# Kernel optimization log

Measured on AMD Instinct MI355X. Metric: run time of the kernel, lower is better.

## Reference

```python
import jax, jax.numpy as jnp
import numpy as np

VOCAB = 100000
DIM = 300
SEQ = 200
BATCH = 1024


def setup_inputs() -> dict:
    key = jax.random.key(0)
    ks = jax.random.split(key, 7)
    tokens = jax.random.randint(ks[0], (SEQ, BATCH), 0, VOCAB, dtype=jnp.int32)
    static_lut = jax.random.normal(ks[1], (VOCAB, DIM), dtype=jnp.float32)
    # lut = pretrained vectors + N(0, 0.01) noise
    lut = static_lut + 0.01 * jax.random.normal(ks[2], (VOCAB, DIM), dtype=jnp.float32)
    W1 = jax.random.normal(ks[3], (600, 600), dtype=jnp.float32) / np.sqrt(600.0)
    b1 = jnp.zeros((600,), dtype=jnp.float32)
    W2 = jax.random.normal(ks[4], (1, 600), dtype=jnp.float32) / np.sqrt(600.0)
    b2 = jnp.zeros((1,), dtype=jnp.float32)
    return {"tokens": tokens, "lut": lut, "static_lut": static_lut,
            "W1": W1, "b1": b1, "W2": W2, "b2": b2}


def _first_occurrence_mask(tokens):
    # tokens: [S, B]. mask[i, b] = 1 iff tokens[i, b] is the first occurrence
    # of that token value in column b (emulates per-column set() dedup).
    S = tokens.shape[0]
    eq = tokens[:, None, :] == tokens[None, :, :]          # [S, S, B]
    first_idx = jnp.argmax(eq, axis=1)                      # [S, B] first j with same token
    return (first_idx == jnp.arange(S, dtype=first_idx.dtype)[:, None])


def reference(tokens, lut, static_lut, W1, b1, W2, b2):
    mask = _first_occurrence_mask(tokens).astype(lut.dtype)  # [S, B]
    # dedup embedding-bag sums over unique tokens per column
    e_learn = jnp.einsum('sbd,sb->bd', lut[tokens], mask)          # [B, 300]
    e_static = jnp.einsum('sbd,sb->bd', static_lut[tokens], mask)  # [B, 300]
    hidden = jnp.concatenate([e_learn, e_static], axis=-1)         # [B, 600]
    h = jax.nn.relu(hidden @ W1.T + b1)                            # [B, 600]
    out = h @ W2.T + b2                                            # [B, 1]
    return out[:, 0]                                               # [B]
```

## Files before the change

### kernel.cpp

```cpp
#include <hip/hip_runtime.h>
#include <limits.h>

#define SEQ   200
#define BATCH 1024
#define DIM   300
#define HID   600
#define VOCAB 100000

#define NQ    4

#define BW    4
#define JCH   12
#define JPER  (HID / JCH)

#define HIDDEN_ELEMS (BATCH * HID)
#define HIDDEN_BYTES ((size_t)HIDDEN_ELEMS * 4)

#define SORT_BYTES  ((size_t)BATCH * 256 * 4)
#define NK_BYTES    ((size_t)BATCH * 4)
#define OFF_NK      SORT_BYTES
#define OFF_HID4    (SORT_BYTES + 65536)
#define OFF_HIDDEN  (OFF_HID4 + 4 * HIDDEN_BYTES)

__global__ __launch_bounds__(256) void sort_kernel(
    const int* __restrict__ tokens,
    int* __restrict__ sorted_g,
    int* __restrict__ nk_g) {
  const int b   = blockIdx.x;
  const int tid = threadIdx.x;

  __shared__ int toks[SEQ];
  __shared__ int stok[256];
  __shared__ int nk_sh;

  for (int s = tid; s < SEQ; s += 256) toks[s] = tokens[s * BATCH + b];
  if (tid == 0) nk_sh = 0;
  __syncthreads();

  int my = INT_MAX;
  if (tid < SEQ) {
    const int t = toks[tid];
    bool k = true;
    for (int p = 0; p < tid; ++p) {
      if (toks[p] == t) { k = false; break; }
    }
    if (k) my = t;
  }
  stok[tid] = my;
  if (my != INT_MAX) atomicAdd(&nk_sh, 1);
  __syncthreads();

  for (int k = 2; k <= 256; k <<= 1) {
    for (int j = k >> 1; j > 0; j >>= 1) {
      const int ixj = tid ^ j;
      if (ixj > tid) {
        const int a = stok[tid];
        const int c = stok[ixj];
        const bool up = ((tid & k) == 0);
        if ((a > c) == up) { stok[tid] = c; stok[ixj] = a; }
      }
      __syncthreads();
    }
  }

  sorted_g[b * 256 + tid] = stok[tid];
  if (tid == 0) nk_g[b] = nk_sh;
}

__global__ __launch_bounds__(192) void embed_gather_kernel(
    const int* __restrict__ sorted_g,
    const int* __restrict__ nk_g,
    const float* __restrict__ lut,
    const float* __restrict__ slut,
    float* __restrict__ hid4) {
  const int b   = blockIdx.x;
  const int q   = blockIdx.y;
  const int tid = threadIdx.x;

  const int nk = nk_g[b];
  const int i0 = (q * nk) / NQ;
  const int i1 = ((q + 1) * nk) / NQ;

  const int tab_i = tid / 75;
  const int slot  = tid % 75;
  if (tab_i < 2) {
    const float* __restrict__ tab = tab_i ? slut : lut;
    const int* __restrict__ rows = sorted_g + b * 256;
    float4 a = make_float4(0.f, 0.f, 0.f, 0.f);
#pragma unroll 8
    for (int i = i0; i < i1; ++i) {
      const float4 v = ((const float4*)(tab + (size_t)rows[i] * DIM))[slot];
      a.x += v.x; a.y += v.y; a.z += v.z; a.w += v.w;
    }
    float* dst = hid4 + ((size_t)q * BATCH + b) * HID + tab_i * DIM;
    ((float4*)dst)[slot] = a;
  }
}

__global__ __launch_bounds__(256) void combine_kernel(
    const float* __restrict__ hid4, float* __restrict__ hidden) {
  const int i = blockIdx.x * 256 + threadIdx.x;
  const int n4 = HIDDEN_ELEMS / 4;
  if (i < n4) {
    const float4* p = (const float4*)hid4;
    const float4 a = p[i];
    const float4 b = p[i + n4];
    const float4 c = p[i + 2 * n4];
    const float4 d = p[i + 3 * n4];
    float4 s;
    s.x = (a.x + b.x) + (c.x + d.x);
    s.y = (a.y + b.y) + (c.y + d.y);
    s.z = (a.z + b.z) + (c.z + d.z);
    s.w = (a.w + b.w) + (c.w + d.w);
    ((float4*)hidden)[i] = s;
  }
}

__global__ __launch_bounds__(256) void out_init_kernel(
    float* __restrict__ out, const float* __restrict__ b2) {
  const int i = blockIdx.x * 256 + threadIdx.x;
  if (i < BATCH) out[i] = b2[0];
}

template <int CTRL>
__device__ __forceinline__ float dpp_add(float x) {
  const int y = __builtin_amdgcn_update_dpp(
      0, __float_as_int(x), CTRL, 0xf, 0xf, true);
  return x + __int_as_float(y);
}

__device__ __forceinline__ float wave_sum(float h) {
  h = dpp_add<0x111>(h);
  h = dpp_add<0x112>(h);
  h = dpp_add<0x114>(h);
  h = dpp_add<0x118>(h);
  h = dpp_add<0x142>(h);
  h = dpp_add<0x143>(h);
  return h;
}

__global__ __launch_bounds__(256) void mlp_kernel(
    const float* __restrict__ hidden,
    const float* __restrict__ W1,
    const float* __restrict__ b1,
    const float* __restrict__ W2,
    float* __restrict__ out) {
  const int wave = threadIdx.x >> 6;
  const int lane = threadIdx.x & 63;
  const int b0   = (blockIdx.x * 4 + wave) * BW;
  const int j0   = blockIdx.y * JPER;

  float a[BW][10];
#pragma unroll
  for (int bb = 0; bb < BW; ++bb) {
    const float* __restrict__ hb = hidden + (size_t)(b0 + bb) * HID;
#pragma unroll
    for (int i = 0; i < 9; ++i) a[bb][i] = hb[lane + 64 * i];
    a[bb][9] = (lane < 24) ? hb[lane + 576] : 0.f;
  }

  float acc[BW] = {0.f, 0.f, 0.f, 0.f};

#pragma unroll 2
  for (int jj = 0; jj < JPER; ++jj) {
    const int j = j0 + jj;
    const float* __restrict__ wr = W1 + (size_t)j * HID;
    float d0 = 0.f, d1 = 0.f, d2 = 0.f, d3 = 0.f;
#pragma unroll
    for (int i = 0; i < 9; ++i) {
      const float w = wr[lane + 64 * i];
      d0 += a[0][i] * w;
      d1 += a[1][i] * w;
      d2 += a[2][i] * w;
      d3 += a[3][i] * w;
    }
    {
      const float w = (lane < 24) ? wr[lane + 576] : 0.f;
      d0 += a[0][9] * w;
      d1 += a[1][9] * w;
      d2 += a[2][9] * w;
      d3 += a[3][9] * w;
    }
    d0 = wave_sum(d0); d1 = wave_sum(d1);
    d2 = wave_sum(d2); d3 = wave_sum(d3);
    const float b1j = b1[j];
    const float w2j = W2[j];
    acc[0] += fmaxf(d0 + b1j, 0.f) * w2j;
    acc[1] += fmaxf(d1 + b1j, 0.f) * w2j;
    acc[2] += fmaxf(d2 + b1j, 0.f) * w2j;
    acc[3] += fmaxf(d3 + b1j, 0.f) * w2j;
  }

  if (lane == 63) {
#pragma unroll
    for (int bb = 0; bb < BW; ++bb) atomicAdd(&out[b0 + bb], acc[bb]);
  }
}

extern "C" void kernel_launch(void* const* d_in, const int* in_sizes, int n_in,
                              void* d_out, int out_size, void* d_ws, size_t ws_size,
                              hipStream_t stream) {
  const int*   tokens = (const int*)  d_in[0];
  const float* lut    = (const float*)d_in[1];
  const float* slut   = (const float*)d_in[2];
  const float* W1     = (const float*)d_in[3];
  const float* b1     = (const float*)d_in[4];
  const float* W2     = (const float*)d_in[5];
  const float* b2     = (const float*)d_in[6];
  float* out = (float*)d_out;

  int*   sorted_g = (int*)d_ws;
  int*   nk_g     = (int*)((char*)d_ws + OFF_NK);
  float* hid4     = (float*)((char*)d_ws + OFF_HID4);
  float* hidden   = (float*)((char*)d_ws + OFF_HIDDEN);

  out_init_kernel<<<(BATCH + 255) / 256, 256, 0, stream>>>(out, b2);
  sort_kernel<<<BATCH, 256, 0, stream>>>(tokens, sorted_g, nk_g);
  embed_gather_kernel<<<dim3(BATCH, NQ), 192, 0, stream>>>(
      sorted_g, nk_g, lut, slut, hid4);
  combine_kernel<<<(HIDDEN_ELEMS / 4 + 255) / 256, 256, 0, stream>>>(
      hid4, hidden);
  mlp_kernel<<<dim3(BATCH / (4 * BW), JCH), 256, 0, stream>>>(
      hidden, W1, b1, W2, out);
}
```

Measured before the change: 131.4 us.

## Replace O(n^2) dedup and bitonic sort with bucketed dedup and compaction

The per-column dedup no longer scans every earlier token and then bitonic-sorts 256 entries. Tokens are now bucketed into 64 value ranges with a shared-memory histogram and prefix scan, and duplicates are checked only within each bucket. Survivors are compacted with a wave-scan prefix sum. This removes the quadratic scan and the many syncthreads of the bitonic network. The output is only bucket-sorted rather than fully sorted, so the gather's row order changes, and the gather loop unroll is raised from 8 to 16.

```diff
diff --git a/kernel.cpp b/kernel.cpp
--- a/kernel.cpp
+++ b/kernel.cpp
@@ -8,6 +8,7 @@
 #define VOCAB 100000
 
 #define NQ    4
+#define NBKT  64
 
 #define BW    4
 #define JCH   12
@@ -17,7 +18,6 @@
 #define HIDDEN_BYTES ((size_t)HIDDEN_ELEMS * 4)
 
 #define SORT_BYTES  ((size_t)BATCH * 256 * 4)
-#define NK_BYTES    ((size_t)BATCH * 4)
 #define OFF_NK      SORT_BYTES
 #define OFF_HID4    (SORT_BYTES + 65536)
 #define OFF_HIDDEN  (OFF_HID4 + 4 * HIDDEN_BYTES)
@@ -26,45 +26,72 @@
     const int* __restrict__ tokens,
     int* __restrict__ sorted_g,
     int* __restrict__ nk_g) {
-  const int b   = blockIdx.x;
-  const int tid = threadIdx.x;
-
-  __shared__ int toks[SEQ];
-  __shared__ int stok[256];
-  __shared__ int nk_sh;
-
-  for (int s = tid; s < SEQ; s += 256) toks[s] = tokens[s * BATCH + b];
-  if (tid == 0) nk_sh = 0;
-  __syncthreads();
-
-  int my = INT_MAX;
+  const int b    = blockIdx.x;
+  const int tid  = threadIdx.x;
+  const int w    = tid >> 6;
+  const int lane = tid & 63;
+
+  __shared__ int hist[NBKT];
+  __shared__ int base[NBKT];
+  __shared__ int cur[NBKT];
+  __shared__ int stok[SEQ];
+  __shared__ int keepf[SEQ];
+  __shared__ int wsum[4];
+
+  if (tid < NBKT) { hist[tid] = 0; cur[tid] = 0; }
+  __syncthreads();
+
+  int t = 0, bk = 0;
   if (tid < SEQ) {
-    const int t = toks[tid];
-    bool k = true;
-    for (int p = 0; p < tid; ++p) {
-      if (toks[p] == t) { k = false; break; }
-    }
-    if (k) my = t;
-  }
-  stok[tid] = my;
-  if (my != INT_MAX) atomicAdd(&nk_sh, 1);
-  __syncthreads();
-
-  for (int k = 2; k <= 256; k <<= 1) {
-    for (int j = k >> 1; j > 0; j >>= 1) {
-      const int ixj = tid ^ j;
-      if (ixj > tid) {
-        const int a = stok[tid];
-        const int c = stok[ixj];
-        const bool up = ((tid & k) == 0);
-        if ((a > c) == up) { stok[tid] = c; stok[ixj] = a; }
-      }
-      __syncthreads();
-    }
-  }
-
-  sorted_g[b * 256 + tid] = stok[tid];
-  if (tid == 0) nk_g[b] = nk_sh;
+    t  = tokens[tid * BATCH + b];
+    bk = (int)((unsigned)t * (unsigned)NBKT / (unsigned)VOCAB);
+    atomicAdd(&hist[bk], 1);
+  }
+  __syncthreads();
+
+  if (tid < NBKT) {
+    const int v = hist[tid];
+    int incl = v;
+#pragma unroll
+    for (int off = 1; off < NBKT; off <<= 1) {
+      const int n = __shfl_up(incl, off, 64);
+      if (lane >= off) incl += n;
+    }
+    base[tid] = incl - v;
+  }
+  __syncthreads();
+
+  int pos = -1;
+  if (tid < SEQ) {
+    pos = base[bk] + atomicAdd(&cur[bk], 1);
+    stok[pos] = t;
+  }
+  __syncthreads();
+
+  if (tid < SEQ) {
+    int kf = 1;
+    const int b0 = base[bk];
+    for (int j = b0; j < pos; ++j) {
+      if (stok[j] == t) { kf = 0; break; }
+    }
+    keepf[pos] = kf;
+  }
+  __syncthreads();
+
+  const int val = (tid < SEQ) ? keepf[tid] : 0;
+  int incl = val;
+#pragma unroll
+  for (int off = 1; off < 64; off <<= 1) {
+    const int n = __shfl_up(incl, off, 64);
+    if (lane >= off) incl += n;
+  }
+  if (lane == 63) wsum[w] = incl;
+  __syncthreads();
+
+  int prefix = 0;
+  for (int q = 0; q < w; ++q) prefix += wsum[q];
+  if (tid < SEQ && val) sorted_g[b * 256 + prefix + incl - val] = stok[tid];
+  if (tid == 0) nk_g[b] = wsum[0] + wsum[1] + wsum[2] + wsum[3];
 }
 
 __global__ __launch_bounds__(192) void embed_gather_kernel(
@@ -87,7 +114,7 @@
     const float* __restrict__ tab = tab_i ? slut : lut;
     const int* __restrict__ rows = sorted_g + b * 256;
     float4 a = make_float4(0.f, 0.f, 0.f, 0.f);
-#pragma unroll 8
+#pragma unroll 16
     for (int i = i0; i < i1; ++i) {
       const float4 v = ((const float4*)(tab + (size_t)rows[i] * DIM))[slot];
       a.x += v.x; a.y += v.y; a.z += v.z; a.w += v.w;
```

Result: faster. 118.6 us (-9.7%).
